# Kernel optimization log

Measured on AMD Instinct MI355X. Metric: run time of the kernel, lower is better.

Reference implementation:

```python
import jax, jax.numpy as jnp
import numpy as np

NUM_NODES = 50000
NUM_EDGES = 640000
H_DIM = 128
OUT_DIM = 128
NUM_RELS = 16
NUM_BASES = 8


def _rgcn_layer(h, basis, coef, bias, src, dst, etype, norm, activation):
    # Basis decomposition: W[r] = sum_b coef[r,b] * basis[b]  -> [R, d_in, d_out]
    W = jnp.einsum('rb,bio->rio', coef, basis)
    # Transform node features under every relation: [R, N, d_out]
    Hr = jnp.einsum('ni,rio->rno', h, W)
    # Per-edge message: pick (relation, source) pair, apply edge norm. [E, d_out]
    msg = Hr[etype, src] * norm
    # Aggregate messages at destination nodes. [N, d_out]
    out = jax.ops.segment_sum(msg, dst, num_segments=h.shape[0])
    out = out + bias
    return activation(out) if activation is not None else out


def setup_inputs() -> dict:
    key = jax.random.key(0)
    ks = jax.random.split(key, 10)
    h = jax.random.normal(ks[0], (NUM_NODES, H_DIM), dtype=jnp.float32)
    norm = jax.random.uniform(ks[1], (NUM_EDGES, 1), dtype=jnp.float32)
    src = jax.random.randint(ks[2], (NUM_EDGES,), 0, NUM_NODES, dtype=jnp.int32)
    dst = jax.random.randint(ks[3], (NUM_EDGES,), 0, NUM_NODES, dtype=jnp.int32)
    etype = jax.random.randint(ks[4], (NUM_EDGES,), 0, NUM_RELS, dtype=jnp.int32)
    s1 = 1.0 / np.sqrt(H_DIM)
    s2 = 1.0 / np.sqrt(H_DIM)
    V1 = jax.random.normal(ks[5], (NUM_BASES, H_DIM, H_DIM), dtype=jnp.float32) * s1
    coef1 = jax.random.normal(ks[6], (NUM_RELS, NUM_BASES), dtype=jnp.float32) * (1.0 / np.sqrt(NUM_BASES))
    bias1 = jnp.zeros((H_DIM,), dtype=jnp.float32)
    V2 = jax.random.normal(ks[7], (NUM_BASES, H_DIM, OUT_DIM), dtype=jnp.float32) * s2
    coef2 = jax.random.normal(ks[8], (NUM_RELS, NUM_BASES), dtype=jnp.float32) * (1.0 / np.sqrt(NUM_BASES))
    bias2 = jnp.zeros((OUT_DIM,), dtype=jnp.float32)
    return {
        'h': h, 'norm': norm, 'src': src, 'dst': dst, 'etype': etype,
        'V1': V1, 'coef1': coef1, 'bias1': bias1,
        'V2': V2, 'coef2': coef2, 'bias2': bias2,
    }


def reference(h, norm, src, dst, etype, V1, coef1, bias1, V2, coef2, bias2):
    # Layer 0: relational graph conv with ReLU (hidden layer)
    h1 = _rgcn_layer(h, V1, coef1, bias1, src, dst, etype, norm, jax.nn.relu)
    # Layer 1+: BaseRGCN sorts edges by relation (bucketing for the low-mem
    # per-relation dispatch). The sort is a permutation of the edge set, so we
    # mirror it explicitly; the segment_sum result is mathematically identical.
    order = jnp.argsort(etype)
    src_s, dst_s, et_s, norm_s = src[order], dst[order], etype[order], norm[order]
    out = _rgcn_layer(h1, V2, coef2, bias2, src_s, dst_s, et_s, norm_s, None)
    return out
```

## Files before the change

kernel.cpp:

```cpp
#include <hip/hip_runtime.h>

#define N_RELS 16
#define N_BASES 8
#define HD 128
#define SCAN_B 1024
#define ROWS 32

typedef __attribute__((ext_vector_type(8))) short bf16x8;
typedef __attribute__((ext_vector_type(4))) float floatx4;
typedef __attribute__((ext_vector_type(2))) float floatx2;

__device__ __forceinline__ short bf16rn(float f) {
    union { float f; unsigned u; } v; v.f = f;
    unsigned u = v.u;
    unsigned r = (u + 0x7fffu + ((u >> 16) & 1u)) >> 16;
    return (short)r;
}


__global__ void setup_fused(const float* __restrict__ h, unsigned* __restrict__ hb, int n4,
                            const float* __restrict__ V1, const float* __restrict__ V2,
                            short* __restrict__ Vf,
                            const int* __restrict__ dst, int E, int* __restrict__ cnt,
                            int packBlocks, int vBlocks) {
    int blk = blockIdx.x;
    if (blk < packBlocks) {
        int i = blk * blockDim.x + threadIdx.x;
        if (i < n4) {
            float4 v = ((const float4*)h)[i];
            uint2 o;
            o.x = ((unsigned)(unsigned short)bf16rn(v.y) << 16) | (unsigned short)bf16rn(v.x);
            o.y = ((unsigned)(unsigned short)bf16rn(v.w) << 16) | (unsigned short)bf16rn(v.z);
            ((uint2*)hb)[i] = o;
        }
        return;
    }
    blk -= packBlocks;
    if (blk < vBlocks) {
        const float* V = ((blk & 8) ? V2 : V1) + (size_t)(blk & 7) * 16384;
        size_t obase = (size_t)blk * 16384;
        for (int e = threadIdx.x; e < 16384; e += blockDim.x) {
            float w = V[e];
            int k = e >> 7, n = e & 127;
            int kk = k >> 5, q = (k >> 3) & 3, j = k & 7;
            int lane = q * 16 + (n & 15);
            int idx = ((kk * 8 + (n >> 4)) * 64 + lane) * 8 + j;
            Vf[obase + idx] = bf16rn(w);
        }
        return;
    }
    blk -= vBlocks;
    int i = blk * blockDim.x + threadIdx.x;
    if (i < E) atomicAdd(&cnt[dst[i]], 1);
}


__global__ void scan_partial(const int* __restrict__ cnt, int N,
                             int* __restrict__ excl, int* __restrict__ bsum) {
    __shared__ int s[SCAN_B];
    int t = threadIdx.x, i = blockIdx.x * SCAN_B + t;
    int v = (i < N) ? cnt[i] : 0;
    s[t] = v; __syncthreads();
    for (int o = 1; o < SCAN_B; o <<= 1) {
        int x = (t >= o) ? s[t - o] : 0;
        __syncthreads();
        s[t] += x;
        __syncthreads();
    }
    if (i < N) excl[i] = s[t] - v;
    if (t == SCAN_B - 1) bsum[blockIdx.x] = s[t];
}

__global__ void scan_fixup(int* __restrict__ row_ptr, const int* __restrict__ bsum,
                           int nb, int N, int E, int* __restrict__ cursor) {
    __shared__ int pref[64];
    int t = threadIdx.x;
    if (t < 64) {
        int raw = (t < nb) ? bsum[t] : 0;
        int v = raw;
#pragma unroll
        for (int o = 1; o < 64; o <<= 1) {
            int u = __shfl_up(v, o, 64);
            if (t >= o) v += u;
        }
        pref[t] = v - raw;
    }
    __syncthreads();
    int i = blockIdx.x * blockDim.x + t;
    if (i < N) { int val = row_ptr[i] + pref[i >> 10]; row_ptr[i] = val; cursor[i] = val; }
    if (i == 0) row_ptr[N] = E;
}

__global__ void scatter_dst(const int* __restrict__ dst, const int* __restrict__ src,
                            const int* __restrict__ et, const float* __restrict__ norm,
                            int E, int* __restrict__ cursor, int2* __restrict__ edata) {
    int i = blockIdx.x * blockDim.x + threadIdx.x;
    if (i >= E) return;
    int p = atomicAdd(&cursor[dst[i]], 1);
    edata[p] = make_int2((et[i] << 16) | src[i], __float_as_int(norm[i]));
}


__global__ __launch_bounds__(512, 4) void rgcn_tile(
    const unsigned* __restrict__ hb, const int2* __restrict__ edata,
    const int* __restrict__ row_ptr, const float* __restrict__ coef,
    const short* __restrict__ Vf, const float* __restrict__ bias,
    void* __restrict__ outp, int N, int E, int mode) {
    __shared__ __align__(16) unsigned Zs[N_BASES][4][4][ROWS + 1][4];

    const int tid = threadIdx.x;
    const int wave = tid >> 6, lane = tid & 63;
    const int nb0 = blockIdx.x * ROWS;

    const int lkk = lane >> 4, lq = (lane >> 2) & 3, lju = lane & 3;

    const int r0 = wave * 4;
    int bounds[5];
#pragma unroll
    for (int i = 0; i < 5; i++) {
        int nd = nb0 + r0 + i; if (nd > N) nd = N;
        bounds[i] = __builtin_amdgcn_readfirstlane(row_ptr[nd]);
    }
    int e = bounds[0];
    const int eend = bounds[4];

    floatx2 acc[N_BASES] = {};
    int cur = 0;

    auto proc = [&](int2 m, unsigned g) {
        int ets = __builtin_amdgcn_readfirstlane(m.x >> 16);
        float nv = __int_as_float(m.y);
        const float* cw = coef + ets * N_BASES;
        floatx2 v;
        v.x = __uint_as_float(g << 16) * nv;
        v.y = __uint_as_float(g & 0xffff0000u) * nv;
#pragma unroll
        for (int b = 0; b < N_BASES; b++)
            acc[b] = v * cw[b] + acc[b];
    };
    auto flush = [&](int r) {
#pragma unroll
        for (int b = 0; b < N_BASES; b++) {
            unsigned lo = (unsigned)(unsigned short)bf16rn(acc[b].x);
            unsigned hi = (unsigned)(unsigned short)bf16rn(acc[b].y);
            Zs[b][lkk][lq][r0 + r][lju] = (hi << 16) | lo;
            acc[b].x = 0.f; acc[b].y = 0.f;
        }
    };

    int2 mb[8];
#pragma unroll
    for (int j = 0; j < 8; j++) { int ix = e + j; if (ix > E - 1) ix = E - 1; mb[j] = edata[ix]; }

    while (e + 8 <= eend) {
        unsigned g[8];
#pragma unroll
        for (int j = 0; j < 8; j++) g[j] = hb[(size_t)(mb[j].x & 0xffff) * 64 + lane];
        int2 nxt[8];
#pragma unroll
        for (int j = 0; j < 8; j++) { int ix = e + 8 + j; if (ix > E - 1) ix = E - 1; nxt[j] = edata[ix]; }
#pragma unroll
        for (int j = 0; j < 8; j++) {
            while (cur < 3 && e + j >= bounds[cur + 1]) { flush(cur); cur++; }
            proc(mb[j], g[j]);
        }
#pragma unroll
        for (int j = 0; j < 8; j++) mb[j] = nxt[j];
        e += 8;
    }
    {
        const int rem = eend - e;
        unsigned g[8];
#pragma unroll
        for (int j = 0; j < 8; j++)
            if (j < rem) g[j] = hb[(size_t)(mb[j].x & 0xffff) * 64 + lane];
#pragma unroll
        for (int j = 0; j < 8; j++)
            if (j < rem) {
                while (cur < 3 && e + j >= bounds[cur + 1]) { flush(cur); cur++; }
                proc(mb[j], g[j]);
            }
    }
    while (cur < 4) { flush(cur); cur++; }

    __syncthreads();

    const int q = lane >> 4, cc = lane & 15;
    const int tt = wave;
    floatx4 ac0 = {}, ac1 = {};

#pragma unroll 2
    for (int b = 0; b < N_BASES; b++) {
#pragma unroll
        for (int kk = 0; kk < 4; kk++) {
            bf16x8 a0 = *(const bf16x8*)&Zs[b][kk][q][cc][0];
            bf16x8 a1 = *(const bf16x8*)&Zs[b][kk][q][16 + cc][0];
            bf16x8 B = *(const bf16x8*)(Vf + (size_t)b * 16384 +
                                        ((size_t)(kk * 8 + tt) * 64 + lane) * 8);
            ac0 = __builtin_amdgcn_mfma_f32_16x16x32_bf16(a0, B, ac0, 0, 0, 0);
            ac1 = __builtin_amdgcn_mfma_f32_16x16x32_bf16(a1, B, ac1, 0, 0, 0);
        }
    }

    float bv = bias[tt * 16 + cc];
    if (mode == 0) {
        unsigned short* o = (unsigned short*)outp;
#pragma unroll
        for (int mi = 0; mi < 2; mi++) {
            const floatx4& c = mi ? ac1 : ac0;
#pragma unroll
            for (int i = 0; i < 4; i++) {
                int node = nb0 + mi * 16 + q * 4 + i;
                if (node < N) {
                    float v = fmaxf(c[i] + bv, 0.f);
                    o[(size_t)node * HD + tt * 16 + cc] = (unsigned short)bf16rn(v);
                }
            }
        }
    } else {
        float* o = (float*)outp;
#pragma unroll
        for (int mi = 0; mi < 2; mi++) {
            const floatx4& c = mi ? ac1 : ac0;
#pragma unroll
            for (int i = 0; i < 4; i++) {
                int node = nb0 + mi * 16 + q * 4 + i;
                if (node < N) o[(size_t)node * HD + tt * 16 + cc] = c[i] + bv;
            }
        }
    }
}


extern "C" void kernel_launch(void* const* d_in, const int* in_sizes, int n_in,
                              void* d_out, int out_size, void* d_ws, size_t ws_size,
                              hipStream_t stream) {
    const float* h     = (const float*)d_in[0];
    const float* norm  = (const float*)d_in[1];
    const int*   src   = (const int*)d_in[2];
    const int*   dst   = (const int*)d_in[3];
    const int*   etype = (const int*)d_in[4];
    const float* V1    = (const float*)d_in[5];
    const float* coef1 = (const float*)d_in[6];
    const float* bias1 = (const float*)d_in[7];
    const float* V2    = (const float*)d_in[8];
    const float* coef2 = (const float*)d_in[9];
    const float* bias2 = (const float*)d_in[10];
    const int N = in_sizes[0] / HD;
    const int E = in_sizes[2];
    float* out = (float*)d_out;
    (void)n_in; (void)out_size; (void)ws_size;

    char* ws = (char*)d_ws;
    size_t off = 0;
    auto alloc = [&](size_t bytes) {
        void* p = ws + off;
        off += (bytes + 255) & ~(size_t)255;
        return p;
    };
    short*    Vf      = (short*)alloc((size_t)16 * 16384 * sizeof(short));
    unsigned* hb      = (unsigned*)alloc((size_t)N * 64 * sizeof(unsigned));
    unsigned* h1b     = (unsigned*)alloc((size_t)N * 64 * sizeof(unsigned));
    int2*     edata   = (int2*)alloc((size_t)E * sizeof(int2));
    int*      cnt     = (int*)alloc((size_t)N * sizeof(int));
    int*      row_ptr = (int*)alloc((size_t)(N + 1) * sizeof(int));
    int*      cursor  = (int*)alloc((size_t)N * sizeof(int));
    int*      bsum    = (int*)alloc(256 * sizeof(int));

    const int nb = (N + SCAN_B - 1) / SCAN_B;
    const int packBlocks = (N * 32 + 255) / 256;
    const int vBlocks = 16;
    const int histBlocks = (E + 255) / 256;

    hipMemsetAsync(cnt, 0, (size_t)N * sizeof(int), stream);
    setup_fused<<<packBlocks + vBlocks + histBlocks, 256, 0, stream>>>(
        h, hb, N * 32, V1, V2, Vf, dst, E, cnt, packBlocks, vBlocks);
    scan_partial<<<nb, SCAN_B, 0, stream>>>(cnt, N, row_ptr, bsum);
    scan_fixup<<<(N + 255) / 256, 256, 0, stream>>>(row_ptr, bsum, nb, N, E, cursor);
    scatter_dst<<<(E + 255) / 256, 256, 0, stream>>>(dst, src, etype, norm, E, cursor, edata);

    const int tiles = (N + ROWS - 1) / ROWS;

    rgcn_tile<<<tiles, 512, 0, stream>>>(hb, edata, row_ptr, coef1, Vf, bias1, h1b, N, E, 0);
    rgcn_tile<<<tiles, 512, 0, stream>>>(h1b, edata, row_ptr, coef2, Vf + (size_t)8 * 16384,
                                         bias2, out, N, E, 1);
}
```

Measured before the change: 329.0 us.

## Assign 16 lanes per destination node with uint4 gathers in aggregation

The edge aggregation loop changes from one wave walking the edges of four nodes sequentially to 16-lane groups, each owning one destination node and gathering 16-byte chunks of the bf16 source row. Relation coefficients are staged in shared memory, and accumulators are packed into Zs with a single vector store per basis. The aim is more edge-level parallelism and fewer serial flush branches. Each wave now iterates to the maximum degree among its four nodes, so lanes on shorter rows do masked zero work, and each thread holds four times as many accumulator registers.

```diff
diff --git a/kernel.cpp b/kernel.cpp
--- a/kernel.cpp
+++ b/kernel.cpp
@@ -15,6 +15,10 @@
     unsigned u = v.u;
     unsigned r = (u + 0x7fffu + ((u >> 16) & 1u)) >> 16;
     return (short)r;
+}
+
+__device__ __forceinline__ unsigned packbf2(floatx2 a) {
+    return ((unsigned)(unsigned short)bf16rn(a.y) << 16) | (unsigned short)bf16rn(a.x);
 }
 
 
@@ -107,82 +111,80 @@
     const short* __restrict__ Vf, const float* __restrict__ bias,
     void* __restrict__ outp, int N, int E, int mode) {
     __shared__ __align__(16) unsigned Zs[N_BASES][4][4][ROWS + 1][4];
+    __shared__ __align__(16) float cofs[N_RELS * N_BASES];
 
     const int tid = threadIdx.x;
     const int wave = tid >> 6, lane = tid & 63;
+    const int l16 = lane & 15;
     const int nb0 = blockIdx.x * ROWS;
 
-    const int lkk = lane >> 4, lq = (lane >> 2) & 3, lju = lane & 3;
-
-    const int r0 = wave * 4;
-    int bounds[5];
-#pragma unroll
-    for (int i = 0; i < 5; i++) {
-        int nd = nb0 + r0 + i; if (nd > N) nd = N;
-        bounds[i] = __builtin_amdgcn_readfirstlane(row_ptr[nd]);
-    }
-    int e = bounds[0];
-    const int eend = bounds[4];
-
-    floatx2 acc[N_BASES] = {};
-    int cur = 0;
-
-    auto proc = [&](int2 m, unsigned g) {
-        int ets = __builtin_amdgcn_readfirstlane(m.x >> 16);
-        float nv = __int_as_float(m.y);
-        const float* cw = coef + ets * N_BASES;
-        floatx2 v;
-        v.x = __uint_as_float(g << 16) * nv;
-        v.y = __uint_as_float(g & 0xffff0000u) * nv;
-#pragma unroll
-        for (int b = 0; b < N_BASES; b++)
-            acc[b] = v * cw[b] + acc[b];
+    if (tid < N_RELS * N_BASES) cofs[tid] = coef[tid];
+    __syncthreads();
+
+    const int r = tid >> 4;
+    const int node = nb0 + (r & 31);
+    const int cn = (node < N) ? node : (N - 1);
+    const int s = row_ptr[cn];
+    const int t = row_ptr[cn + 1];
+    const int len = (node < N) ? (t - s) : 0;
+
+    int mx = len;
+    mx = max(mx, __shfl_xor(mx, 16, 64));
+    mx = max(mx, __shfl_xor(mx, 32, 64));
+    const int nG = __builtin_amdgcn_readfirstlane(mx);
+
+    floatx2 acc[4][N_BASES] = {};
+
+    auto edix = [&](int j) { int ix = s + j; return (ix > E - 1) ? (E - 1) : ix; };
+    auto gath = [&](int2 m) {
+        return ((const uint4*)(hb + (size_t)(m.x & 0xffff) * 64))[l16];
     };
-    auto flush = [&](int r) {
+    auto procG = [&](int2 m, uint4 g, int j) {
+        float nv = (j < len) ? __int_as_float(m.y) : 0.f;
+        int ets = m.x >> 16;
+        floatx4 c0 = *(const floatx4*)&cofs[ets * 8];
+        floatx4 c1 = *(const floatx4*)&cofs[ets * 8 + 4];
+        floatx2 v0, v1, v2, v3;
+        v0.x = __uint_as_float(g.x << 16) * nv; v0.y = __uint_as_float(g.x & 0xffff0000u) * nv;
+        v1.x = __uint_as_float(g.y << 16) * nv; v1.y = __uint_as_float(g.y & 0xffff0000u) * nv;
+        v2.x = __uint_as_float(g.z << 16) * nv; v2.y = __uint_as_float(g.z & 0xffff0000u) * nv;
+        v3.x = __uint_as_float(g.w << 16) * nv; v3.y = __uint_as_float(g.w & 0xffff0000u) * nv;
 #pragma unroll
         for (int b = 0; b < N_BASES; b++) {
-            unsigned lo = (unsigned)(unsigned short)bf16rn(acc[b].x);
-            unsigned hi = (unsigned)(unsigned short)bf16rn(acc[b].y);
-            Zs[b][lkk][lq][r0 + r][lju] = (hi << 16) | lo;
-            acc[b].x = 0.f; acc[b].y = 0.f;
+            float cw = (b < 4) ? c0[b & 3] : c1[b & 3];
+            acc[0][b] = v0 * cw + acc[0][b];
+            acc[1][b] = v1 * cw + acc[1][b];
+            acc[2][b] = v2 * cw + acc[2][b];
+            acc[3][b] = v3 * cw + acc[3][b];
         }
     };
 
-    int2 mb[8];
-#pragma unroll
-    for (int j = 0; j < 8; j++) { int ix = e + j; if (ix > E - 1) ix = E - 1; mb[j] = edata[ix]; }
-
-    while (e + 8 <= eend) {
-        unsigned g[8];
-#pragma unroll
-        for (int j = 0; j < 8; j++) g[j] = hb[(size_t)(mb[j].x & 0xffff) * 64 + lane];
-        int2 nxt[8];
-#pragma unroll
-        for (int j = 0; j < 8; j++) { int ix = e + 8 + j; if (ix > E - 1) ix = E - 1; nxt[j] = edata[ix]; }
-#pragma unroll
-        for (int j = 0; j < 8; j++) {
-            while (cur < 3 && e + j >= bounds[cur + 1]) { flush(cur); cur++; }
-            proc(mb[j], g[j]);
-        }
-#pragma unroll
-        for (int j = 0; j < 8; j++) mb[j] = nxt[j];
-        e += 8;
-    }
+    int2 m0 = edata[edix(0)];
+    uint4 g0 = gath(m0);
+    int2 m1 = edata[edix(1)];
+
+    int k = 0;
+    for (; k + 2 <= nG; k += 2) {
+        uint4 g1 = gath(m1);
+        procG(m0, g0, k);
+        m0 = edata[edix(k + 2)];
+        g0 = gath(m0);
+        procG(m1, g1, k + 1);
+        m1 = edata[edix(k + 3)];
+    }
+    if (k < nG) procG(m0, g0, k);
+
     {
-        const int rem = eend - e;
-        unsigned g[8];
-#pragma unroll
-        for (int j = 0; j < 8; j++)
-            if (j < rem) g[j] = hb[(size_t)(mb[j].x & 0xffff) * 64 + lane];
-#pragma unroll
-        for (int j = 0; j < 8; j++)
-            if (j < rem) {
-                while (cur < 3 && e + j >= bounds[cur + 1]) { flush(cur); cur++; }
-                proc(mb[j], g[j]);
-            }
-    }
-    while (cur < 4) { flush(cur); cur++; }
-
+        uint4 w;
+#pragma unroll
+        for (int b = 0; b < N_BASES; b++) {
+            w.x = packbf2(acc[0][b]);
+            w.y = packbf2(acc[1][b]);
+            w.z = packbf2(acc[2][b]);
+            w.w = packbf2(acc[3][b]);
+            *(uint4*)&Zs[b][l16 >> 2][l16 & 3][r & 31][0] = w;
+        }
+    }
     __syncthreads();
 
     const int q = lane >> 4, cc = lane & 15;
@@ -210,10 +212,10 @@
             const floatx4& c = mi ? ac1 : ac0;
 #pragma unroll
             for (int i = 0; i < 4; i++) {
-                int node = nb0 + mi * 16 + q * 4 + i;
-                if (node < N) {
+                int nd = nb0 + mi * 16 + q * 4 + i;
+                if (nd < N) {
                     float v = fmaxf(c[i] + bv, 0.f);
-                    o[(size_t)node * HD + tt * 16 + cc] = (unsigned short)bf16rn(v);
+                    o[(size_t)nd * HD + tt * 16 + cc] = (unsigned short)bf16rn(v);
                 }
             }
         }
@@ -224,8 +226,8 @@
             const floatx4& c = mi ? ac1 : ac0;
 #pragma unroll
             for (int i = 0; i < 4; i++) {
-                int node = nb0 + mi * 16 + q * 4 + i;
-                if (node < N) o[(size_t)node * HD + tt * 16 + cc] = c[i] + bv;
+                int nd = nb0 + mi * 16 + q * 4 + i;
+                if (nd < N) o[(size_t)nd * HD + tt * 16 + cc] = c[i] + bv;
             }
         }
     }
```

Result: faster. 304.6 us (-7.4%).
